# Kernel tuning notes

Hardware: AMD Instinct MI355X
Metric: run time of the kernel (lower is better)

Reference implementation:

```python
import jax, jax.numpy as jnp
import numpy as np
from math import ceil, log2

N_ROWS, M_COLS = 4096, 4096
LEVELS, FILT_LEN = 8, 16


def circ_conv(a, b, n):
    # circular convolution of each row of a with filter b, both zero-padded/truncated to length n
    return jnp.fft.irfft(jnp.fft.rfft(a, n=n) * jnp.fft.rfft(b, n=n), n=n)


def forward_level(x, w):
    # one forward DWT step over rows of x using wavelet filter w
    part = x.shape[1] // 2
    g = jnp.flip(w).at[1::2].multiply(-1.0)  # scaling filter g_k = (-1)^k h_{M-k-1}
    we, wo = w[::2], w[1::2]
    ge, go = g[::2], g[1::2]
    even, odd = x[:, ::2], x[:, 1::2]
    details = circ_conv(even, we, part) + circ_conv(odd, wo, part)
    approx = circ_conv(even, ge, part) + circ_conv(odd, go, part)
    return details, approx


def backward_level(details, approx, w):
    # one inverse DWT step: zero-upsample then circular-convolve with synthesis filters
    ws = jnp.flip(w)                       # wavelet synthesis
    ss = w.at[1::2].multiply(-1.0)         # scaling synthesis
    n, md = details.shape
    fd = jnp.zeros((n, 2 * md), details.dtype).at[:, ::2].set(details)
    fa = jnp.zeros((n, 2 * approx.shape[1]), approx.dtype).at[:, ::2].set(approx)
    return circ_conv(fd, ws, 2 * md) + circ_conv(fa, ss, 2 * approx.shape[1])


def despawn(x, wavelet):
    input_length = x.shape[1]
    target = 2 ** ceil(log2(input_length))
    x = jnp.pad(x, ((0, 0), (0, target - input_length)), mode='edge')  # ReplicationPad1d
    levels = wavelet.shape[0]
    approx = x
    coeffs = []
    for lvl in range(levels):
        d, approx = forward_level(approx, wavelet[lvl])
        coeffs.append(d)
    coeffs.append(approx)
    # inverse transform (note: original applies no thresholding in forward)
    rec = coeffs[-1]
    for lvl in reversed(range(levels)):
        rec = backward_level(coeffs[lvl], rec, wavelet[lvl])
    return rec[:, :input_length], jnp.concatenate(coeffs, axis=-1)


def setup_inputs() -> dict:
    key = jax.random.key(0)
    k1, k2 = jax.random.split(key)
    inp = jax.random.normal(k1, (N_ROWS, M_COLS), dtype=jnp.float32)
    wavelet = jax.random.normal(k2, (LEVELS, FILT_LEN), dtype=jnp.float32) * 0.3
    return {"input": inp, "wavelet": wavelet}


def reference(input, wavelet):
    return despawn(input, wavelet)
```

## Files before the change

kernel.cpp:

```cpp
#include <hip/hip_runtime.h>

#define NROWS 4096
#define NCOLS 4096
#define TPB   256


#define LD4(arr, base, vec) { float4 _v = (vec); (arr)[(base)] = _v.x; (arr)[(base)+1] = _v.y; (arr)[(base)+2] = _v.z; (arr)[(base)+3] = _v.w; }
#define LD2(arr, base, vec) { float2 _v = (vec); (arr)[(base)] = _v.x; (arr)[(base)+1] = _v.y; }

#define WAVE_FENCE() do { asm volatile("s_waitcnt lgkmcnt(0)" ::: "memory"); \
                          __builtin_amdgcn_sched_barrier(0); } while (0)

__device__ __forceinline__ void fwd_pt(const float* e8, const float* o8,
                                       const float* wl, float& dd, float& aa)
{
    float d = 0.f, a = 0.f;
    #pragma unroll
    for (int t = 0; t < 8; ++t) {
        float e = e8[-t], o = o8[-t];
        d = fmaf(wl[2*t],     e, d);
        d = fmaf(wl[2*t+1],   o, d);
        a = fmaf(wl[15-2*t],  e, a);
        a = fmaf(-wl[14-2*t], o, a);
    }
    dd = d; aa = a;
}

__device__ __forceinline__ void fwd_pt2(const float* e8, const float* o8,
                                        const float* wl, float& dd, float& aa)
{
    float d = 0.f, a = 0.f;
    #pragma unroll
    for (int t = 0; t < 8; ++t) {
        float e = e8[-2*t], o = o8[-2*t];
        d = fmaf(wl[2*t],     e, d);
        d = fmaf(wl[2*t+1],   o, d);
        a = fmaf(wl[15-2*t],  e, a);
        a = fmaf(-wl[14-2*t], o, a);
    }
    dd = d; aa = a;
}

__device__ __forceinline__ void bwd_pt(const float* d8, const float* a8,
                                       const float* wl, float& rr0, float& rr1)
{
    float x = 0.f, y = 0.f;
    #pragma unroll
    for (int t = 0; t < 8; ++t) {
        float dv = d8[-t], av = a8[-t];
        x = fmaf(wl[15-2*t], dv, x);
        x = fmaf(wl[2*t],    av, x);
        y = fmaf(wl[14-2*t], dv, y);
        y = fmaf(-wl[2*t+1], av, y);
    }
    rr0 = x; rr1 = y;
}

__global__ __launch_bounds__(TPB, 6) void despawn_kernel(
    const float* __restrict__ in, const float* __restrict__ wv,
    float* __restrict__ out_rec, float* __restrict__ out_coef)
{
    __shared__ float P0[2048];
    __shared__ float P1[2048];
    __shared__ float Csm[512];

    const int tid = threadIdx.x;
    const int row = blockIdx.x;
    const float* rowIn = in + (size_t)row * NCOLS;
    float* crow = out_coef + (size_t)row * NCOLS;
    float* rrow = out_rec  + (size_t)row * NCOLS;

    float wl[16];

    {
        #pragma unroll
        for (int q = 0; q < 16; ++q) wl[q] = wv[q];
        const float4* X4 = (const float4*)rowIn;
        const int k0 = tid * 8;
        {
            float xw[24];
            #pragma unroll
            for (int j = 0; j < 6; ++j) LD4(xw, 4*j, X4[(4*tid - 4 + j) & 1023]);
            float d[4], a[4];
            #pragma unroll
            for (int p = 0; p < 4; ++p) fwd_pt2(&xw[16 + 2*p], &xw[17 + 2*p], wl, d[p], a[p]);
            *(float4*)(crow + k0) = make_float4(d[0], d[1], d[2], d[3]);
            *(float2*)(P0 + (k0 >> 1))        = make_float2(a[0], a[2]);
            *(float2*)(P0 + 1024 + (k0 >> 1)) = make_float2(a[1], a[3]);
        }
        {
            float xw[24];
            #pragma unroll
            for (int j = 0; j < 6; ++j) LD4(xw, 4*j, X4[(4*tid - 2 + j) & 1023]);
            float d[4], a[4];
            #pragma unroll
            for (int p = 0; p < 4; ++p) fwd_pt2(&xw[16 + 2*p], &xw[17 + 2*p], wl, d[p], a[p]);
            *(float4*)(crow + k0 + 4) = make_float4(d[0], d[1], d[2], d[3]);
            *(float2*)(P0 + (k0 >> 1) + 2)        = make_float2(a[0], a[2]);
            *(float2*)(P0 + 1024 + (k0 >> 1) + 2) = make_float2(a[1], a[3]);
        }
    }
    __syncthreads();

    {
        #pragma unroll
        for (int q = 0; q < 16; ++q) wl[q] = wv[16 + q];
        const float4* E4 = (const float4*)P0;
        const float4* O4 = (const float4*)(P0 + 1024);
        float xe[12], xo[12];
        #pragma unroll
        for (int j = 0; j < 3; ++j) {
            int idx = (tid - 2 + j) & 255;
            LD4(xe, 4*j, E4[idx]); LD4(xo, 4*j, O4[idx]);
        }
        float d[4], a[4];
        #pragma unroll
        for (int p = 0; p < 4; ++p) fwd_pt(&xe[8 + p], &xo[8 + p], wl, d[p], a[p]);
        const int k0 = tid * 4;
        *(float4*)(crow + 2048 + k0) = make_float4(d[0], d[1], d[2], d[3]);
        *(float2*)(P1 + (k0 >> 1))       = make_float2(a[0], a[2]);
        *(float2*)(P1 + 512 + (k0 >> 1)) = make_float2(a[1], a[3]);
    }
    __syncthreads();

    {
        #pragma unroll
        for (int q = 0; q < 16; ++q) wl[q] = wv[32 + q];
        const float2* Ev = (const float2*)P1;
        const float2* Ov = (const float2*)(P1 + 512);
        float xe[10], xo[10];
        #pragma unroll
        for (int j = 0; j < 5; ++j) {
            int idx = (tid - 4 + j) & 255;
            LD2(xe, 2*j, Ev[idx]); LD2(xo, 2*j, Ov[idx]);
        }
        float d[2], a[2];
        #pragma unroll
        for (int p = 0; p < 2; ++p) fwd_pt(&xe[8 + p], &xo[8 + p], wl, d[p], a[p]);
        const int k0 = tid * 2;
        *(float2*)(crow + 3072 + k0) = make_float2(d[0], d[1]);
        P0[tid]       = a[0];
        P0[256 + tid] = a[1];
    }
    __syncthreads();

    if (tid < 64) {
        const float* Ein = P0;
        float* aout = P0 + 512;
        int part = 256, cs = 0, cg = 3584;
        for (int lvl = 3; lvl < 8; ++lvl) {
            #pragma unroll
            for (int q = 0; q < 16; ++q) wl[q] = wv[16*lvl + q];
            const int nth = part >> 2;
            if (tid < nth) {
                const int pm = nth - 1;
                const float4* E4 = (const float4*)Ein;
                const float4* O4 = (const float4*)(Ein + part);
                float xe[12], xo[12];
                #pragma unroll
                for (int j = 0; j < 3; ++j) {
                    int idx = (tid - 2 + j) & pm;
                    LD4(xe, 4*j, E4[idx]); LD4(xo, 4*j, O4[idx]);
                }
                float d[4], a[4];
                #pragma unroll
                for (int p = 0; p < 4; ++p) fwd_pt(&xe[8 + p], &xo[8 + p], wl, d[p], a[p]);
                const int k0 = tid * 4;
                float4 dv = make_float4(d[0], d[1], d[2], d[3]);
                *(float4*)(Csm + cs + k0)  = dv;
                *(float4*)(crow + cg + k0) = dv;
                if (lvl == 7) {
                    float4 av = make_float4(a[0], a[1], a[2], a[3]);
                    *(float4*)(Csm + 496 + k0)   = av;
                    *(float4*)(crow + 4080 + k0) = av;
                } else {
                    *(float2*)(aout + (k0 >> 1))               = make_float2(a[0], a[2]);
                    *(float2*)(aout + (part >> 1) + (k0 >> 1)) = make_float2(a[1], a[3]);
                }
            }
            WAVE_FENCE();
            Ein = aout; aout += part; cs += part; cg += part; part >>= 1;
        }
        const float* A = Csm + 496;
        float* outp = P0 + 1024;
        int md = 16, dOff = 480;
        for (int lvl = 7; lvl >= 3; --lvl) {
            #pragma unroll
            for (int q = 0; q < 16; ++q) wl[q] = wv[16*lvl + q];
            const int nth = md >> 2;
            if (tid < nth) {
                const int pm = nth - 1;
                const float4* D4 = (const float4*)(Csm + dOff);
                const float4* A4 = (const float4*)A;
                float xd[12], xa[12];
                #pragma unroll
                for (int j = 0; j < 3; ++j) {
                    int idx = (tid - 2 + j) & pm;
                    LD4(xd, 4*j, D4[idx]); LD4(xa, 4*j, A4[idx]);
                }
                float r0[4], r1[4];
                #pragma unroll
                for (int p = 0; p < 4; ++p) bwd_pt(&xd[8 + p], &xa[8 + p], wl, r0[p], r1[p]);
                const int j0 = tid * 4;
                ((float4*)(outp + 2*j0))[0] = make_float4(r0[0], r1[0], r0[1], r1[1]);
                ((float4*)(outp + 2*j0))[1] = make_float4(r0[2], r1[2], r0[3], r1[3]);
            }
            WAVE_FENCE();
            A = outp; outp += 2*md; md <<= 1; dOff -= md;
        }
    }
    __syncthreads();

    {
        #pragma unroll
        for (int q = 0; q < 16; ++q) wl[q] = wv[32 + q];
        const float2* Dg = (const float2*)(crow + 3072);
        const float2* Av = (const float2*)(P0 + 1504);
        float xd[10], xa[10];
        #pragma unroll
        for (int j = 0; j < 5; ++j) {
            int idx = (tid - 4 + j) & 255;
            LD2(xd, 2*j, Dg[idx]); LD2(xa, 2*j, Av[idx]);
        }
        float r0[2], r1[2];
        #pragma unroll
        for (int p = 0; p < 2; ++p) bwd_pt(&xd[8 + p], &xa[8 + p], wl, r0[p], r1[p]);
        const int j0 = tid * 2;
        *(float4*)(P0 + 2*j0) = make_float4(r0[0], r1[0], r0[1], r1[1]);
    }
    __syncthreads();

    {
        #pragma unroll
        for (int q = 0; q < 16; ++q) wl[q] = wv[16 + q];
        const float4* Dg = (const float4*)(crow + 2048);
        const float4* Av = (const float4*)P0;
        float xd[12], xa[12];
        #pragma unroll
        for (int j = 0; j < 3; ++j) {
            int idx = (tid - 2 + j) & 255;
            LD4(xd, 4*j, Dg[idx]); LD4(xa, 4*j, Av[idx]);
        }
        float r0[4], r1[4];
        #pragma unroll
        for (int p = 0; p < 4; ++p) bwd_pt(&xd[8 + p], &xa[8 + p], wl, r0[p], r1[p]);
        const int j0 = tid * 4;
        ((float4*)(P1 + 2*j0))[0] = make_float4(r0[0], r1[0], r0[1], r1[1]);
        ((float4*)(P1 + 2*j0))[1] = make_float4(r0[2], r1[2], r0[3], r1[3]);
    }
    __syncthreads();

    {
        #pragma unroll
        for (int q = 0; q < 16; ++q) wl[q] = wv[q];
        const float4* Dg = (const float4*)crow;
        const float4* Av = (const float4*)P1;
        const int j0 = tid * 8;
        {
            float xd[12], xa[12];
            #pragma unroll
            for (int c = 0; c < 3; ++c) {
                int idx = (2*tid - 2 + c) & 511;
                LD4(xd, 4*c, Dg[idx]); LD4(xa, 4*c, Av[idx]);
            }
            float r0[4], r1[4];
            #pragma unroll
            for (int p = 0; p < 4; ++p) bwd_pt(&xd[8 + p], &xa[8 + p], wl, r0[p], r1[p]);
            ((float4*)(rrow + 2*j0))[0] = make_float4(r0[0], r1[0], r0[1], r1[1]);
            ((float4*)(rrow + 2*j0))[1] = make_float4(r0[2], r1[2], r0[3], r1[3]);
        }
        {
            float xd[12], xa[12];
            #pragma unroll
            for (int c = 0; c < 3; ++c) {
                int idx = (2*tid - 1 + c) & 511;
                LD4(xd, 4*c, Dg[idx]); LD4(xa, 4*c, Av[idx]);
            }
            float r0[4], r1[4];
            #pragma unroll
            for (int p = 0; p < 4; ++p) bwd_pt(&xd[8 + p], &xa[8 + p], wl, r0[p], r1[p]);
            ((float4*)(rrow + 2*j0))[2] = make_float4(r0[0], r1[0], r0[1], r1[1]);
            ((float4*)(rrow + 2*j0))[3] = make_float4(r0[2], r1[2], r0[3], r1[3]);
        }
    }
}

extern "C" void kernel_launch(void* const* d_in, const int* in_sizes, int n_in,
                              void* d_out, int out_size, void* d_ws, size_t ws_size,
                              hipStream_t stream) {
    (void)in_sizes; (void)n_in; (void)d_ws; (void)ws_size; (void)out_size;
    const float* in = (const float*)d_in[0];
    const float* wv = (const float*)d_in[1];
    float* out_rec  = (float*)d_out;
    float* out_coef = (float*)d_out + (size_t)NROWS * NCOLS;
    despawn_kernel<<<NROWS, TPB, 0, stream>>>(in, wv, out_rec, out_coef);
}
```

Baseline: 56.83 us.

## Keep detail coefficients in LDS for inverse pass instead of reloading global

```diff
diff --git a/kernel.cpp b/kernel.cpp
--- a/kernel.cpp
+++ b/kernel.cpp
@@ -7,9 +7,6 @@
 
 #define LD4(arr, base, vec) { float4 _v = (vec); (arr)[(base)] = _v.x; (arr)[(base)+1] = _v.y; (arr)[(base)+2] = _v.z; (arr)[(base)+3] = _v.w; }
 #define LD2(arr, base, vec) { float2 _v = (vec); (arr)[(base)] = _v.x; (arr)[(base)+1] = _v.y; }
-
-#define WAVE_FENCE() do { asm volatile("s_waitcnt lgkmcnt(0)" ::: "memory"); \
-                          __builtin_amdgcn_sched_barrier(0); } while (0)
 
 __device__ __forceinline__ void fwd_pt(const float* e8, const float* o8,
                                        const float* wl, float& dd, float& aa)
@@ -56,13 +53,16 @@
     rr0 = x; rr1 = y;
 }
 
-__global__ __launch_bounds__(TPB, 6) void despawn_kernel(
+__global__ __launch_bounds__(TPB, 5) void despawn_kernel(
     const float* __restrict__ in, const float* __restrict__ wv,
     float* __restrict__ out_rec, float* __restrict__ out_coef)
 {
     __shared__ float P0[2048];
-    __shared__ float P1[2048];
+    __shared__ float P1[1024];
     __shared__ float Csm[512];
+    __shared__ float D0[2048];
+    __shared__ float D1[1024];
+    __shared__ float D2[512];
 
     const int tid = threadIdx.x;
     const int row = blockIdx.x;
@@ -76,29 +76,21 @@
         #pragma unroll
         for (int q = 0; q < 16; ++q) wl[q] = wv[q];
         const float4* X4 = (const float4*)rowIn;
+        float xw[32];
+        #pragma unroll
+        for (int j = 0; j < 8; ++j) LD4(xw, 4*j, X4[(4*tid - 4 + j) & 1023]);
+        float d[8], a[8];
+        #pragma unroll
+        for (int p = 0; p < 8; ++p) fwd_pt2(&xw[16 + 2*p], &xw[17 + 2*p], wl, d[p], a[p]);
         const int k0 = tid * 8;
-        {
-            float xw[24];
-            #pragma unroll
-            for (int j = 0; j < 6; ++j) LD4(xw, 4*j, X4[(4*tid - 4 + j) & 1023]);
-            float d[4], a[4];
-            #pragma unroll
-            for (int p = 0; p < 4; ++p) fwd_pt2(&xw[16 + 2*p], &xw[17 + 2*p], wl, d[p], a[p]);
-            *(float4*)(crow + k0) = make_float4(d[0], d[1], d[2], d[3]);
-            *(float2*)(P0 + (k0 >> 1))        = make_float2(a[0], a[2]);
-            *(float2*)(P0 + 1024 + (k0 >> 1)) = make_float2(a[1], a[3]);
-        }
-        {
-            float xw[24];
-            #pragma unroll
-            for (int j = 0; j < 6; ++j) LD4(xw, 4*j, X4[(4*tid - 2 + j) & 1023]);
-            float d[4], a[4];
-            #pragma unroll
-            for (int p = 0; p < 4; ++p) fwd_pt2(&xw[16 + 2*p], &xw[17 + 2*p], wl, d[p], a[p]);
-            *(float4*)(crow + k0 + 4) = make_float4(d[0], d[1], d[2], d[3]);
-            *(float2*)(P0 + (k0 >> 1) + 2)        = make_float2(a[0], a[2]);
-            *(float2*)(P0 + 1024 + (k0 >> 1) + 2) = make_float2(a[1], a[3]);
-        }
+        float4 d0v = make_float4(d[0], d[1], d[2], d[3]);
+        float4 d1v = make_float4(d[4], d[5], d[6], d[7]);
+        ((float4*)(crow + k0))[0] = d0v;
+        ((float4*)(crow + k0))[1] = d1v;
+        ((float4*)(D0 + k0))[0]   = d0v;
+        ((float4*)(D0 + k0))[1]   = d1v;
+        *(float4*)(P0 + (k0 >> 1))        = make_float4(a[0], a[2], a[4], a[6]);
+        *(float4*)(P0 + 1024 + (k0 >> 1)) = make_float4(a[1], a[3], a[5], a[7]);
     }
     __syncthreads();
 
@@ -117,7 +109,9 @@
         #pragma unroll
         for (int p = 0; p < 4; ++p) fwd_pt(&xe[8 + p], &xo[8 + p], wl, d[p], a[p]);
         const int k0 = tid * 4;
-        *(float4*)(crow + 2048 + k0) = make_float4(d[0], d[1], d[2], d[3]);
+        float4 dv = make_float4(d[0], d[1], d[2], d[3]);
+        *(float4*)(crow + 2048 + k0) = dv;
+        *(float4*)(D1 + k0)          = dv;
         *(float2*)(P1 + (k0 >> 1))       = make_float2(a[0], a[2]);
         *(float2*)(P1 + 512 + (k0 >> 1)) = make_float2(a[1], a[3]);
     }
@@ -138,13 +132,15 @@
         #pragma unroll
         for (int p = 0; p < 2; ++p) fwd_pt(&xe[8 + p], &xo[8 + p], wl, d[p], a[p]);
         const int k0 = tid * 2;
-        *(float2*)(crow + 3072 + k0) = make_float2(d[0], d[1]);
+        float2 dv = make_float2(d[0], d[1]);
+        *(float2*)(crow + 3072 + k0) = dv;
+        *(float2*)(D2 + k0)          = dv;
         P0[tid]       = a[0];
         P0[256 + tid] = a[1];
     }
     __syncthreads();
 
-    if (tid < 64) {
+    {
         const float* Ein = P0;
         float* aout = P0 + 512;
         int part = 256, cs = 0, cg = 3584;
@@ -178,10 +174,13 @@
                     *(float2*)(aout + (part >> 1) + (k0 >> 1)) = make_float2(a[1], a[3]);
                 }
             }
-            WAVE_FENCE();
+            __syncthreads();
             Ein = aout; aout += part; cs += part; cg += part; part >>= 1;
         }
-        const float* A = Csm + 496;
+    }
+
+    const float* A = Csm + 496;
+    {
         float* outp = P0 + 1024;
         int md = 16, dOff = 480;
         for (int lvl = 7; lvl >= 3; --lvl) {
@@ -205,16 +204,15 @@
                 ((float4*)(outp + 2*j0))[0] = make_float4(r0[0], r1[0], r0[1], r1[1]);
                 ((float4*)(outp + 2*j0))[1] = make_float4(r0[2], r1[2], r0[3], r1[3]);
             }
-            WAVE_FENCE();
+            __syncthreads();
             A = outp; outp += 2*md; md <<= 1; dOff -= md;
         }
     }
-    __syncthreads();
 
     {
         #pragma unroll
         for (int q = 0; q < 16; ++q) wl[q] = wv[32 + q];
-        const float2* Dg = (const float2*)(crow + 3072);
+        const float2* Dg = (const float2*)D2;
         const float2* Av = (const float2*)(P0 + 1504);
         float xd[10], xa[10];
         #pragma unroll
@@ -226,15 +224,15 @@
         #pragma unroll
         for (int p = 0; p < 2; ++p) bwd_pt(&xd[8 + p], &xa[8 + p], wl, r0[p], r1[p]);
         const int j0 = tid * 2;
-        *(float4*)(P0 + 2*j0) = make_float4(r0[0], r1[0], r0[1], r1[1]);
+        *(float4*)(P1 + 2*j0) = make_float4(r0[0], r1[0], r0[1], r1[1]);
     }
     __syncthreads();
 
     {
         #pragma unroll
         for (int q = 0; q < 16; ++q) wl[q] = wv[16 + q];
-        const float4* Dg = (const float4*)(crow + 2048);
-        const float4* Av = (const float4*)P0;
+        const float4* Dg = (const float4*)D1;
+        const float4* Av = (const float4*)P1;
         float xd[12], xa[12];
         #pragma unroll
         for (int j = 0; j < 3; ++j) {
@@ -245,16 +243,16 @@
         #pragma unroll
         for (int p = 0; p < 4; ++p) bwd_pt(&xd[8 + p], &xa[8 + p], wl, r0[p], r1[p]);
         const int j0 = tid * 4;
-        ((float4*)(P1 + 2*j0))[0] = make_float4(r0[0], r1[0], r0[1], r1[1]);
-        ((float4*)(P1 + 2*j0))[1] = make_float4(r0[2], r1[2], r0[3], r1[3]);
+        ((float4*)(P0 + 2*j0))[0] = make_float4(r0[0], r1[0], r0[1], r1[1]);
+        ((float4*)(P0 + 2*j0))[1] = make_float4(r0[2], r1[2], r0[3], r1[3]);
     }
     __syncthreads();
 
     {
         #pragma unroll
         for (int q = 0; q < 16; ++q) wl[q] = wv[q];
-        const float4* Dg = (const float4*)crow;
-        const float4* Av = (const float4*)P1;
+        const float4* Dg = (const float4*)D0;
+        const float4* Av = (const float4*)P0;
         const int j0 = tid * 8;
         {
             float xd[12], xa[12];
```

Result: no change. 56.53 us (-0.5%).
